# Performance work log

Measured on AMD Instinct MI355X. Metric: run time of the kernel, lower is better.

Reference implementation:

```python
import jax, jax.numpy as jnp
import numpy as np

N_NODES = 50000
N_EDGES = 800000
IN_F = 128
HEADS = 8
D_HEAD = 16  # out_features // num_heads = 128 // 8


def setup_inputs() -> dict:
    key = jax.random.key(0)
    k1, k2, k3, k4, k5 = jax.random.split(key, 5)
    x = jax.random.normal(k1, (N_NODES, IN_F), dtype=jnp.float32)
    edge_index = jax.random.randint(k2, (2, N_EDGES), 0, N_NODES, dtype=jnp.int64)
    # nn.Linear weight is [out, in]; xavier-ish scale
    W = jax.random.normal(k3, (HEADS * D_HEAD, IN_F), dtype=jnp.float32) * (1.0 / np.sqrt(IN_F))
    a_src = jax.random.normal(k4, (HEADS, D_HEAD), dtype=jnp.float32) * (1.0 / np.sqrt(D_HEAD))
    a_dst = jax.random.normal(k5, (HEADS, D_HEAD), dtype=jnp.float32) * (1.0 / np.sqrt(D_HEAD))
    return {"x": x, "edge_index": edge_index, "W": W, "a_src": a_src, "a_dst": a_dst}


def reference(x, edge_index, W, a_src, a_dst):
    N = x.shape[0]
    H, D = a_src.shape
    # h = W x, reshaped to [N, H, D]
    h = (x @ W.T).reshape(N, H, D)
    src, dst = edge_index[0], edge_index[1]
    # per-node attention logits, then gather per-edge (same math as gathering h first)
    s_src = jnp.einsum("nhd,hd->nh", h, a_src)  # [N, H]
    s_dst = jnp.einsum("nhd,hd->nh", h, a_dst)  # [N, H]
    attn = jax.nn.leaky_relu(s_src[src] + s_dst[dst], negative_slope=0.2)  # [E, H]
    # torch scatter_reduce amax onto a zeros tensor -> max is clamped at 0
    attn_max = jnp.maximum(jax.ops.segment_max(attn, dst, num_segments=N), 0.0)  # [N, H]
    e = jnp.exp(attn - attn_max[dst])  # [E, H]
    attn_sum = jax.ops.segment_sum(e, dst, num_segments=N)  # [N, H]
    alpha = e / (attn_sum[dst] + 1e-10)  # [E, H] (dropout is identity in eval)
    msg = h[src] * alpha[..., None]  # [E, H, D]
    out = jax.ops.segment_sum(msg, dst, num_segments=N)  # [N, H, D]
    return out.reshape(N, H * D)
```

## Files before the change

kernel.cpp:

```cpp
#include <hip/hip_runtime.h>
#include <hip/hip_bf16.h>

#define N_NODES 50000
#define N_EDGES 800000
#define HEADS 8
#define MAXDEG 64
#define NPB 4
#define NMFMA ((N_NODES + 127) / 128)
#define NBINB 391
#define NBUCK 128
#define BUCK_NODES 391
#define BUCK_CAP 12288

using frag_ab = __attribute__((ext_vector_type(8))) short;
using frag_cd = __attribute__((ext_vector_type(4))) float;

static __device__ __forceinline__ short f2bs(float v) {
    __hip_bfloat16 b = __float2bfloat16(v);
    return *(short*)&b;
}

__global__ __launch_bounds__(256) void k_fm(const float* __restrict__ x,
                                            const float* __restrict__ W,
                                            const float* __restrict__ a_src,
                                            const float* __restrict__ a_dst,
                                            __hip_bfloat16* __restrict__ hb,
                                            float* __restrict__ s_src,
                                            float* __restrict__ s_dst,
                                            const int* __restrict__ ei,
                                            int* __restrict__ gcount,
                                            int2* __restrict__ bbuf) {
    __shared__ short Ws[144][136];
    const int t = threadIdx.x;

    if (blockIdx.x >= NMFMA) {
        __shared__ int hist[NBUCK];
        __shared__ int basei[NBUCK];
        const int fb = blockIdx.x - NMFMA;
        for (int i = t; i < NBUCK; i += 256) hist[i] = 0;
        __syncthreads();

        const int e0 = fb * 2048 + t * 8;
        const bool active = (e0 + 8 <= N_EDGES);
        int srcs[8], dsts[8], bks[8];
        if (active) {
            int4 s0 = *(const int4*)(ei + e0);
            int4 s1 = *(const int4*)(ei + e0 + 4);
            int4 d0 = *(const int4*)(ei + N_EDGES + e0);
            int4 d1 = *(const int4*)(ei + N_EDGES + e0 + 4);
            srcs[0] = s0.x; srcs[1] = s0.y; srcs[2] = s0.z; srcs[3] = s0.w;
            srcs[4] = s1.x; srcs[5] = s1.y; srcs[6] = s1.z; srcs[7] = s1.w;
            dsts[0] = d0.x; dsts[1] = d0.y; dsts[2] = d0.z; dsts[3] = d0.w;
            dsts[4] = d1.x; dsts[5] = d1.y; dsts[6] = d1.z; dsts[7] = d1.w;
            #pragma unroll
            for (int u = 0; u < 8; ++u) {
                bks[u] = dsts[u] / BUCK_NODES;
                atomicAdd(&hist[bks[u]], 1);
            }
        }
        __syncthreads();
        if (t < NBUCK) {
            int h = hist[t];
            basei[t] = h ? atomicAdd(&gcount[t], h) : 0;
            hist[t] = 0;
        }
        __syncthreads();
        if (active) {
            #pragma unroll
            for (int u = 0; u < 8; ++u) {
                int off = atomicAdd(&hist[bks[u]], 1);
                int pos = basei[bks[u]] + off;
                if (pos < BUCK_CAP)
                    bbuf[bks[u] * BUCK_CAP + pos] = make_int2(srcs[u], dsts[u]);
            }
        }
        return;
    }

    for (int i = t; i < 128 * 16; i += 256) {
        int r = i >> 4, c = (i & 15) << 3;
        float4 w0 = *(const float4*)(W + r * 128 + c);
        float4 w1 = *(const float4*)(W + r * 128 + c + 4);
        frag_ab v;
        v[0] = f2bs(w0.x); v[1] = f2bs(w0.y); v[2] = f2bs(w0.z); v[3] = f2bs(w0.w);
        v[4] = f2bs(w1.x); v[5] = f2bs(w1.y); v[6] = f2bs(w1.z); v[7] = f2bs(w1.w);
        *(frag_ab*)&Ws[r][c] = v;
    }
    for (int i = t; i < 16 * 128; i += 256) {
        int rr = i >> 7, k = i & 127;
        int hd = rr & 7;
        const float* av = (rr < 8) ? a_src : a_dst;
        float v = 0.f;
        #pragma unroll
        for (int d = 0; d < 16; ++d)
            v += av[hd * 16 + d] * W[(size_t)(hd * 16 + d) * 128 + k];
        Ws[128 + rr][k] = f2bs(v);
    }
    __syncthreads();

    const int wave = t >> 6, lane = t & 63;
    const int rb0 = blockIdx.x * 128 + wave * 16;
    if (rb0 >= N_NODES) return;
    const int rb1 = rb0 + 64;
    const int m16 = lane & 15, kg = lane >> 4;
    const int arow0 = min(rb0 + m16, N_NODES - 1);
    const int arow1 = min(rb1 + m16, N_NODES - 1);
    const float* ab0 = x + (size_t)arow0 * 128 + kg * 8;
    const float* ab1 = x + (size_t)arow1 * 128 + kg * 8;

    frag_cd acc[2][9];
    #pragma unroll
    for (int r = 0; r < 2; ++r)
        #pragma unroll
        for (int j = 0; j < 9; ++j) acc[r][j] = (frag_cd){0.f, 0.f, 0.f, 0.f};

    #pragma unroll
    for (int ks = 0; ks < 4; ++ks) {
        float4 p0 = *(const float4*)(ab0 + ks * 32);
        float4 p1 = *(const float4*)(ab0 + ks * 32 + 4);
        float4 q0 = *(const float4*)(ab1 + ks * 32);
        float4 q1 = *(const float4*)(ab1 + ks * 32 + 4);
        frag_ab af0, af1;
        af0[0] = f2bs(p0.x); af0[1] = f2bs(p0.y); af0[2] = f2bs(p0.z); af0[3] = f2bs(p0.w);
        af0[4] = f2bs(p1.x); af0[5] = f2bs(p1.y); af0[6] = f2bs(p1.z); af0[7] = f2bs(p1.w);
        af1[0] = f2bs(q0.x); af1[1] = f2bs(q0.y); af1[2] = f2bs(q0.z); af1[3] = f2bs(q0.w);
        af1[4] = f2bs(q1.x); af1[5] = f2bs(q1.y); af1[6] = f2bs(q1.z); af1[7] = f2bs(q1.w);
        #pragma unroll
        for (int nt = 0; nt < 9; ++nt) {
            frag_ab bf = *(const frag_ab*)&Ws[nt * 16 + m16][ks * 32 + kg * 8];
            acc[0][nt] = __builtin_amdgcn_mfma_f32_16x16x32_bf16(af0, bf, acc[0][nt], 0, 0, 0);
            acc[1][nt] = __builtin_amdgcn_mfma_f32_16x16x32_bf16(af1, bf, acc[1][nt], 0, 0, 0);
        }
    }

    #pragma unroll
    for (int r = 0; r < 2; ++r) {
        int rbase = r ? rb1 : rb0;
        #pragma unroll
        for (int nt = 0; nt < 9; ++nt) {
            #pragma unroll
            for (int j = 0; j < 4; ++j) {
                int row = rbase + kg * 4 + j;
                if (row >= N_NODES) continue;
                int col = nt * 16 + m16;
                float v = acc[r][nt][j];
                if (col < 128)      hb[(size_t)row * 128 + col] = __float2bfloat16(v);
                else if (col < 136) s_src[row * 8 + (col - 128)] = v;
                else                s_dst[row * 8 + (col - 136)] = v;
            }
        }
    }
}

__global__ __launch_bounds__(256) void k_ell(const int2* __restrict__ bbuf,
                                             const int* __restrict__ gcount,
                                             int* __restrict__ cursor,
                                             int* __restrict__ csr_ell) {
    __shared__ int cur[BUCK_NODES];
    const int b = blockIdx.x;
    const int t = threadIdx.x;
    const int lo = b * BUCK_NODES;
    const int hi = min(lo + BUCK_NODES, N_NODES);
    const int ncur = hi - lo;
    for (int i = t; i < ncur; i += 256) cur[i] = 0;
    __syncthreads();
    const int cnt = min(gcount[b], BUCK_CAP);
    for (int i = t; i < cnt; i += 256) {
        int2 e = bbuf[(size_t)b * BUCK_CAP + i];
        int pos = atomicAdd(&cur[e.y - lo], 1);
        if (pos < MAXDEG) csr_ell[e.y * MAXDEG + pos] = e.x;
    }
    __syncthreads();
    for (int i = t; i < ncur; i += 256) cursor[lo + i] = cur[i];
}

__global__ __launch_bounds__(256) void k_gather(const int* __restrict__ csr_ell,
                                                const int* __restrict__ cursor,
                                                const float* __restrict__ s_src,
                                                const float* __restrict__ s_dst,
                                                const __hip_bfloat16* __restrict__ hb,
                                                float* __restrict__ out) {
    __shared__ int   csr_l[NPB][MAXDEG];
    __shared__ float sa[NPB][MAXDEG][9];
    const int slot = threadIdx.x >> 6;
    const int lane = threadIdx.x & 63;
    const int n = blockIdx.x * NPB + slot;
    if (n >= N_NODES) return;
    const int hd8 = lane >> 3, l8 = lane & 7;
    const int deg = min(cursor[n], MAXDEG);
    const int degPad = (deg + 15) & ~15;
    const float sdst = s_dst[n * 8 + hd8];

    if (lane < degPad) csr_l[slot][lane] = (lane < deg) ? csr_ell[n * MAXDEG + lane] : 0;

    float s = 0.f;
    for (int j = l8; j < deg; j += 8) {
        float a = s_src[csr_l[slot][j] * 8 + hd8] + sdst;
        a = a > 0.f ? a : 0.2f * a;
        float w = __expf(a);
        sa[slot][j][hd8] = w;
        s += w;
    }
    for (int j = deg + hd8; j < degPad; j += 8)
        sa[slot][j][l8] = 0.f;
    #pragma unroll
    for (int mask = 1; mask <= 4; mask <<= 1)
        s += __shfl_xor(s, mask);
    float rcp = 1.0f / (s + 1e-10f);

    const int q = lane >> 4;
    const int fl = lane & 15;
    const int hd = fl >> 1;
    const float rcpq = __shfl(rcp, hd * 8);

    const unsigned short* hbs = (const unsigned short*)hb;
    float acc[8] = {0.f, 0.f, 0.f, 0.f, 0.f, 0.f, 0.f, 0.f};

    const int nIter = degPad >> 4;
    for (int it = 0; it < nIter; ++it) {
        const int j = it << 4;
        int  jj0 = j + q,      jj1 = j + 4 + q,  jj2 = j + 8 + q,  jj3 = j + 12 + q;
        int  s0 = csr_l[slot][jj0], s1 = csr_l[slot][jj1];
        int  s2 = csr_l[slot][jj2], s3 = csr_l[slot][jj3];
        float w0 = sa[slot][jj0][hd], w1 = sa[slot][jj1][hd];
        float w2 = sa[slot][jj2][hd], w3 = sa[slot][jj3][hd];
        uint4 v0 = *(const uint4*)(hbs + (size_t)s0 * 128 + fl * 8);
        uint4 v1 = *(const uint4*)(hbs + (size_t)s1 * 128 + fl * 8);
        uint4 v2 = *(const uint4*)(hbs + (size_t)s2 * 128 + fl * 8);
        uint4 v3 = *(const uint4*)(hbs + (size_t)s3 * 128 + fl * 8);
        #define ACC8(vv, ww) \
            acc[0] += (ww) * __uint_as_float((vv).x << 16); \
            acc[1] += (ww) * __uint_as_float((vv).x & 0xffff0000u); \
            acc[2] += (ww) * __uint_as_float((vv).y << 16); \
            acc[3] += (ww) * __uint_as_float((vv).y & 0xffff0000u); \
            acc[4] += (ww) * __uint_as_float((vv).z << 16); \
            acc[5] += (ww) * __uint_as_float((vv).z & 0xffff0000u); \
            acc[6] += (ww) * __uint_as_float((vv).w << 16); \
            acc[7] += (ww) * __uint_as_float((vv).w & 0xffff0000u);
        ACC8(v0, w0) ACC8(v1, w1) ACC8(v2, w2) ACC8(v3, w3)
        #undef ACC8
    }

    #pragma unroll
    for (int k = 0; k < 8; ++k) {
        acc[k] += __shfl_xor(acc[k], 16);
        acc[k] += __shfl_xor(acc[k], 32);
    }
    if (q == 0) {
        float4 o0 = { acc[0] * rcpq, acc[1] * rcpq, acc[2] * rcpq, acc[3] * rcpq };
        float4 o1 = { acc[4] * rcpq, acc[5] * rcpq, acc[6] * rcpq, acc[7] * rcpq };
        *(float4*)(out + (size_t)n * 128 + fl * 8)     = o0;
        *(float4*)(out + (size_t)n * 128 + fl * 8 + 4) = o1;
    }
}

extern "C" void kernel_launch(void* const* d_in, const int* in_sizes, int n_in,
                              void* d_out, int out_size, void* d_ws, size_t ws_size,
                              hipStream_t stream) {
    const float* x     = (const float*)d_in[0];
    const int*   ei    = (const int*)d_in[1];
    const float* W     = (const float*)d_in[2];
    const float* a_src = (const float*)d_in[3];
    const float* a_dst = (const float*)d_in[4];
    float* out = (float*)d_out;

    char* ws = (char*)d_ws;
    __hip_bfloat16* hb      = (__hip_bfloat16*)(ws);
    float*          s_src   = (float*)(ws + 12800000);
    float*          s_dst   = (float*)(ws + 14400000);
    int*            cursor  = (int*)  (ws + 16000000);
    int*            gcount  = (int*)  (ws + 16200000);
    int*            csr_ell = (int*)  (ws + 16200512);
    int2*           bbuf    = (int2*) (ws + 29000512);

    hipMemsetAsync(gcount, 0, NBUCK * 4, stream);
    k_fm    <<<NMFMA + NBINB, 256, 0, stream>>>(x, W, a_src, a_dst, hb, s_src, s_dst, ei, gcount, bbuf);
    k_ell   <<<NBUCK, 256, 0, stream>>>(bbuf, gcount, cursor, csr_ell);
    k_gather<<<(N_NODES + NPB - 1) / NPB, 256, 0, stream>>>(csr_ell, cursor, s_src, s_dst, hb, out);
}
```

Baseline: 85.32 us.

## Fuse attention weight computation into gather loop, drop shared score buffer

```diff
diff --git a/kernel.cpp b/kernel.cpp
--- a/kernel.cpp
+++ b/kernel.cpp
@@ -18,6 +18,9 @@
 static __device__ __forceinline__ short f2bs(float v) {
     __hip_bfloat16 b = __float2bfloat16(v);
     return *(short*)&b;
+}
+static __device__ __forceinline__ float bs2f(short s) {
+    return __uint_as_float(((unsigned)(unsigned short)s) << 16);
 }
 
 __global__ __launch_bounds__(256) void k_fm(const float* __restrict__ x,
@@ -31,6 +34,7 @@
                                             int* __restrict__ gcount,
                                             int2* __restrict__ bbuf) {
     __shared__ short Ws[144][136];
+    __shared__ float asd[256];
     const int t = threadIdx.x;
 
     if (blockIdx.x >= NMFMA) {
@@ -77,6 +81,7 @@
         return;
     }
 
+    if (t < 128) { asd[t] = a_src[t]; asd[128 + t] = a_dst[t]; }
     for (int i = t; i < 128 * 16; i += 256) {
         int r = i >> 4, c = (i & 15) << 3;
         float4 w0 = *(const float4*)(W + r * 128 + c);
@@ -86,14 +91,15 @@
         v[4] = f2bs(w1.x); v[5] = f2bs(w1.y); v[6] = f2bs(w1.z); v[7] = f2bs(w1.w);
         *(frag_ab*)&Ws[r][c] = v;
     }
+    __syncthreads();
     for (int i = t; i < 16 * 128; i += 256) {
         int rr = i >> 7, k = i & 127;
         int hd = rr & 7;
-        const float* av = (rr < 8) ? a_src : a_dst;
+        const float* av = asd + ((rr < 8) ? 0 : 128) + hd * 16;
         float v = 0.f;
         #pragma unroll
         for (int d = 0; d < 16; ++d)
-            v += av[hd * 16 + d] * W[(size_t)(hd * 16 + d) * 128 + k];
+            v += av[d] * bs2f(Ws[hd * 16 + d][k]);
         Ws[128 + rr][k] = f2bs(v);
     }
     __syncthreads();
@@ -107,6 +113,7 @@
     const int arow1 = min(rb1 + m16, N_NODES - 1);
     const float* ab0 = x + (size_t)arow0 * 128 + kg * 8;
     const float* ab1 = x + (size_t)arow1 * 128 + kg * 8;
+    const bool full = (blockIdx.x * 128 + 128 <= N_NODES);
 
     frag_cd acc[2][9];
     #pragma unroll
@@ -141,7 +148,7 @@
             #pragma unroll
             for (int j = 0; j < 4; ++j) {
                 int row = rbase + kg * 4 + j;
-                if (row >= N_NODES) continue;
+                if (!full && row >= N_NODES) continue;
                 int col = nt * 16 + m16;
                 float v = acc[r][nt][j];
                 if (col < 128)      hb[(size_t)row * 128 + col] = __float2bfloat16(v);
@@ -180,54 +187,48 @@
                                                 const float* __restrict__ s_dst,
                                                 const __hip_bfloat16* __restrict__ hb,
                                                 float* __restrict__ out) {
-    __shared__ int   csr_l[NPB][MAXDEG];
-    __shared__ float sa[NPB][MAXDEG][9];
+    __shared__ int csr_l[NPB][MAXDEG];
     const int slot = threadIdx.x >> 6;
     const int lane = threadIdx.x & 63;
     const int n = blockIdx.x * NPB + slot;
     if (n >= N_NODES) return;
-    const int hd8 = lane >> 3, l8 = lane & 7;
     const int deg = min(cursor[n], MAXDEG);
     const int degPad = (deg + 15) & ~15;
-    const float sdst = s_dst[n * 8 + hd8];
 
     if (lane < degPad) csr_l[slot][lane] = (lane < deg) ? csr_ell[n * MAXDEG + lane] : 0;
-
-    float s = 0.f;
-    for (int j = l8; j < deg; j += 8) {
-        float a = s_src[csr_l[slot][j] * 8 + hd8] + sdst;
-        a = a > 0.f ? a : 0.2f * a;
-        float w = __expf(a);
-        sa[slot][j][hd8] = w;
-        s += w;
-    }
-    for (int j = deg + hd8; j < degPad; j += 8)
-        sa[slot][j][l8] = 0.f;
-    #pragma unroll
-    for (int mask = 1; mask <= 4; mask <<= 1)
-        s += __shfl_xor(s, mask);
-    float rcp = 1.0f / (s + 1e-10f);
 
     const int q = lane >> 4;
     const int fl = lane & 15;
     const int hd = fl >> 1;
-    const float rcpq = __shfl(rcp, hd * 8);
+    const float sdst = s_dst[n * 8 + hd];
 
     const unsigned short* hbs = (const unsigned short*)hb;
+    float s = 0.f;
     float acc[8] = {0.f, 0.f, 0.f, 0.f, 0.f, 0.f, 0.f, 0.f};
 
     const int nIter = degPad >> 4;
     for (int it = 0; it < nIter; ++it) {
         const int j = it << 4;
-        int  jj0 = j + q,      jj1 = j + 4 + q,  jj2 = j + 8 + q,  jj3 = j + 12 + q;
-        int  s0 = csr_l[slot][jj0], s1 = csr_l[slot][jj1];
-        int  s2 = csr_l[slot][jj2], s3 = csr_l[slot][jj3];
-        float w0 = sa[slot][jj0][hd], w1 = sa[slot][jj1][hd];
-        float w2 = sa[slot][jj2][hd], w3 = sa[slot][jj3][hd];
+        int jj0 = j + q, jj1 = j + 4 + q, jj2 = j + 8 + q, jj3 = j + 12 + q;
+        int s0 = csr_l[slot][jj0], s1 = csr_l[slot][jj1];
+        int s2 = csr_l[slot][jj2], s3 = csr_l[slot][jj3];
+        float a0 = s_src[s0 * 8 + hd] + sdst;
+        float a1 = s_src[s1 * 8 + hd] + sdst;
+        float a2 = s_src[s2 * 8 + hd] + sdst;
+        float a3 = s_src[s3 * 8 + hd] + sdst;
+        a0 = a0 > 0.f ? a0 : 0.2f * a0;
+        a1 = a1 > 0.f ? a1 : 0.2f * a1;
+        a2 = a2 > 0.f ? a2 : 0.2f * a2;
+        a3 = a3 > 0.f ? a3 : 0.2f * a3;
+        float w0 = (jj0 < deg) ? __expf(a0) : 0.f;
+        float w1 = (jj1 < deg) ? __expf(a1) : 0.f;
+        float w2 = (jj2 < deg) ? __expf(a2) : 0.f;
+        float w3 = (jj3 < deg) ? __expf(a3) : 0.f;
         uint4 v0 = *(const uint4*)(hbs + (size_t)s0 * 128 + fl * 8);
         uint4 v1 = *(const uint4*)(hbs + (size_t)s1 * 128 + fl * 8);
         uint4 v2 = *(const uint4*)(hbs + (size_t)s2 * 128 + fl * 8);
         uint4 v3 = *(const uint4*)(hbs + (size_t)s3 * 128 + fl * 8);
+        s += w0 + w1 + w2 + w3;
         #define ACC8(vv, ww) \
             acc[0] += (ww) * __uint_as_float((vv).x << 16); \
             acc[1] += (ww) * __uint_as_float((vv).x & 0xffff0000u); \
@@ -241,14 +242,19 @@
         #undef ACC8
     }
 
+    s += __shfl_xor(s, 1);
+    s += __shfl_xor(s, 16);
+    s += __shfl_xor(s, 32);
+    const float rcp = 2.0f / (s + 2e-10f);
+
     #pragma unroll
     for (int k = 0; k < 8; ++k) {
         acc[k] += __shfl_xor(acc[k], 16);
         acc[k] += __shfl_xor(acc[k], 32);
     }
     if (q == 0) {
-        float4 o0 = { acc[0] * rcpq, acc[1] * rcpq, acc[2] * rcpq, acc[3] * rcpq };
-        float4 o1 = { acc[4] * rcpq, acc[5] * rcpq, acc[6] * rcpq, acc[7] * rcpq };
+        float4 o0 = { acc[0] * rcp, acc[1] * rcp, acc[2] * rcp, acc[3] * rcp };
+        float4 o1 = { acc[4] * rcp, acc[5] * rcp, acc[6] * rcp, acc[7] * rcp };
         *(float4*)(out + (size_t)n * 128 + fl * 8)     = o0;
         *(float4*)(out + (size_t)n * 128 + fl * 8 + 4) = o1;
     }
```

New measurement: 81.29 us. -4.7%, faster.
